# Optimization experiments

Measured on AMD Instinct MI355X. Metric: run time of the kernel, lower is better.

The kernel has to match this reference:

```python
import jax, jax.numpy as jnp
import numpy as np

NEG_INF = -1e25


def setup_inputs() -> dict:
    key = jax.random.key(0)
    ks = jax.random.split(key, 7)
    B, L, Q, H = 4, 512, 64, 768
    bert = jax.random.normal(ks[0], (B, L, H), dtype=jnp.float32)
    query = jax.random.normal(ks[1], (B, Q, H), dtype=jnp.float32)
    mask = jax.random.randint(ks[2], (B, L), 0, 2).astype(bool)
    # nn.Linear(2H, H): weight (H, 2H), bias (H)
    W_w = jax.random.normal(ks[3], (H, 2 * H), dtype=jnp.float32) * (1.0 / np.sqrt(2 * H))
    W_b = jax.random.normal(ks[4], (H,), dtype=jnp.float32) * 0.02
    # nn.Linear(H, 1): weight (1, H), bias (1)
    v_w = jax.random.normal(ks[5], (1, H), dtype=jnp.float32) * (1.0 / np.sqrt(H))
    v_b = jax.random.normal(ks[6], (1,), dtype=jnp.float32) * 0.02
    return {"bert": bert, "query": query, "mask": mask,
            "W_w": W_w, "W_b": W_b, "v_w": v_w, "v_b": v_b}


def reference(bert, query, mask, W_w, W_b, v_w, v_b):
    H = bert.shape[-1]
    # Linear(cat([bert, query])) = bert @ Wb^T + query @ Wq^T + b  (avoids the (B,Q,L,2H) concat)
    W_bert = W_w[:, :H]    # (H, H) acts on bert part
    W_query = W_w[:, H:]   # (H, H) acts on query part
    bp = jnp.einsum('blh,kh->blk', bert, W_bert)     # (B, L, H)
    qp = jnp.einsum('bqh,kh->bqk', query, W_query)   # (B, Q, H)
    h = jnp.tanh(bp[:, None, :, :] + qp[:, :, None, :] + W_b)  # (B, Q, L, H)
    x = jnp.einsum('bqlh,h->bql', h, v_w[0]) + v_b[0]           # (B, Q, L)
    x = jnp.where(mask[:, None, :], x, NEG_INF)
    return jax.nn.softmax(x, axis=-1)
```

## Files before the change

### kernel.cpp

```cpp
#include <hip/hip_runtime.h>
#include <hip/hip_bf16.h>

#define LOG2E    1.4426950408889634f
#define TWOLOG2E 2.8853900817779268f

typedef short bf16x8 __attribute__((ext_vector_type(8)));
typedef float f32x4  __attribute__((ext_vector_type(4)));
typedef unsigned short u16x8 __attribute__((ext_vector_type(8)));

static __device__ __forceinline__ float bf16_to_f(unsigned short u) {
    union { unsigned int i; float f; } v; v.i = ((unsigned int)u) << 16; return v.f;
}
static __device__ __forceinline__ unsigned short f_to_bf16_rne(float x) {
    union { float f; unsigned int i; } v; v.f = x;
    unsigned int lsb = (v.i >> 16) & 1u;
    v.i += 0x7fffu + lsb;
    return (unsigned short)(v.i >> 16);
}

__global__ __launch_bounds__(256) void cast_frag(
    const float* __restrict__ bert, const float* __restrict__ query,
    const float* __restrict__ Ww,
    unsigned short* __restrict__ Ahf, unsigned short* __restrict__ Alf,
    unsigned short* __restrict__ Whf, unsigned short* __restrict__ Wlf)
{
    const int i    = blockIdx.x * 256 + threadIdx.x;
    const int lane = i & 63;
    const float* src;
    float scale;
    unsigned short *dh, *dl;
    size_t di;
    if (i < 221184) {
        const int rest = i >> 6;
        const int kt = rest % 24, mt = rest / 24;
        const int m  = mt * 16 + (lane & 15);
        src = ((m < 2048) ? bert + (size_t)m * 768
                          : query + (size_t)(m - 2048) * 768)
              + kt * 32 + (lane >> 4) * 8;
        scale = 1.0f;
        dh = Ahf; dl = Alf; di = (size_t)i * 8;
    } else {
        const int j = i - 221184;
        const int rest = j >> 6;
        const int kt = rest % 24, nt2 = rest / 24;
        const int sel = (nt2 >= 48) ? 1 : 0;
        const int n   = (nt2 - sel * 48) * 16 + (lane & 15);
        src = Ww + (size_t)n * 1536 + sel * 768 + kt * 32 + (lane >> 4) * 8;
        scale = TWOLOG2E;
        dh = Whf; dl = Wlf; di = (size_t)j * 8;
    }
    float4 x0 = *(const float4*)src;
    float4 x1 = *(const float4*)(src + 4);
    float xs[8] = {x0.x * scale, x0.y * scale, x0.z * scale, x0.w * scale,
                   x1.x * scale, x1.y * scale, x1.z * scale, x1.w * scale};
    u16x8 h, l;
    #pragma unroll
    for (int e = 0; e < 8; ++e) {
        unsigned short hh = f_to_bf16_rne(xs[e]);
        h[e] = hh;
        l[e] = f_to_bf16_rne(xs[e] - bf16_to_f(hh));
    }
    *(u16x8*)(dh + di) = h;
    *(u16x8*)(dl + di) = l;
}

__global__ __launch_bounds__(64) void gemm_frag(
    const unsigned short* __restrict__ Ahf, const unsigned short* __restrict__ Alf,
    const unsigned short* __restrict__ Whf, const unsigned short* __restrict__ Wlf,
    const float* __restrict__ Wb, float* __restrict__ bpT, float* __restrict__ qp)
{
    const int l    = threadIdx.x;
    const int w    = blockIdx.x;
    const int mt_w = w / 24;
    const int nt_w = w % 24;
    const int m0   = mt_w * 32;
    const int n0   = nt_w * 32;
    const bool isq = (m0 >= 2048);
    const int  fmt = mt_w * 2;
    const int  fnt = (isq ? 48 : 0) + nt_w * 2;
    const int  lr  = l & 15;
    const int  kg  = l >> 4;

    const unsigned short* pAh = Ahf + (size_t)fmt * 12288 + l * 8;
    const unsigned short* pAl = Alf + (size_t)fmt * 12288 + l * 8;
    const unsigned short* pBh = Whf + (size_t)fnt * 12288 + l * 8;
    const unsigned short* pBl = Wlf + (size_t)fnt * 12288 + l * 8;

    f32x4 acc[2][2];
    #pragma unroll
    for (int i = 0; i < 2; ++i)
        #pragma unroll
        for (int j = 0; j < 2; ++j) acc[i][j] = (f32x4){0.f, 0.f, 0.f, 0.f};

    if (!isq) {
        #pragma unroll 4
        for (int kt = 0; kt < 24; ++kt) {
            bf16x8 ah[2], al[2], bh[2], bl[2];
            #pragma unroll
            for (int i = 0; i < 2; ++i) {
                ah[i] = *(const bf16x8*)(pAh + (size_t)i * 12288 + kt * 512);
                al[i] = *(const bf16x8*)(pAl + (size_t)i * 12288 + kt * 512);
                bh[i] = *(const bf16x8*)(pBh + (size_t)i * 12288 + kt * 512);
                bl[i] = *(const bf16x8*)(pBl + (size_t)i * 12288 + kt * 512);
            }
            #pragma unroll
            for (int i = 0; i < 2; ++i)
                #pragma unroll
                for (int j = 0; j < 2; ++j) {
                    acc[i][j] = __builtin_amdgcn_mfma_f32_16x16x32_bf16(bh[i], ah[j], acc[i][j], 0, 0, 0);
                    acc[i][j] = __builtin_amdgcn_mfma_f32_16x16x32_bf16(bh[i], al[j], acc[i][j], 0, 0, 0);
                    acc[i][j] = __builtin_amdgcn_mfma_f32_16x16x32_bf16(bl[i], ah[j], acc[i][j], 0, 0, 0);
                }
        }
        #pragma unroll
        for (int i = 0; i < 2; ++i)
            #pragma unroll
            for (int j = 0; j < 2; ++j)
                #pragma unroll
                for (int r = 0; r < 4; ++r) {
                    const int nrow = n0 + i * 16 + kg * 4 + r;
                    const int mcol = m0 + j * 16 + lr;
                    bpT[(size_t)nrow * 2048 + mcol] = acc[i][j][r];
                }
    } else {
        #pragma unroll 4
        for (int kt = 0; kt < 24; ++kt) {
            bf16x8 ah[2], al[2], bh[2], bl[2];
            #pragma unroll
            for (int i = 0; i < 2; ++i) {
                ah[i] = *(const bf16x8*)(pAh + (size_t)i * 12288 + kt * 512);
                al[i] = *(const bf16x8*)(pAl + (size_t)i * 12288 + kt * 512);
                bh[i] = *(const bf16x8*)(pBh + (size_t)i * 12288 + kt * 512);
                bl[i] = *(const bf16x8*)(pBl + (size_t)i * 12288 + kt * 512);
            }
            #pragma unroll
            for (int i = 0; i < 2; ++i)
                #pragma unroll
                for (int j = 0; j < 2; ++j) {
                    acc[i][j] = __builtin_amdgcn_mfma_f32_16x16x32_bf16(ah[i], bh[j], acc[i][j], 0, 0, 0);
                    acc[i][j] = __builtin_amdgcn_mfma_f32_16x16x32_bf16(ah[i], bl[j], acc[i][j], 0, 0, 0);
                    acc[i][j] = __builtin_amdgcn_mfma_f32_16x16x32_bf16(al[i], bh[j], acc[i][j], 0, 0, 0);
                }
        }
        #pragma unroll
        for (int j = 0; j < 2; ++j) {
            const int col  = n0 + j * 16 + lr;
            const float bias = Wb[col] * TWOLOG2E;
            #pragma unroll
            for (int i = 0; i < 2; ++i)
                #pragma unroll
                for (int r = 0; r < 4; ++r) {
                    const int row = m0 - 2048 + i * 16 + kg * 4 + r;
                    qp[(size_t)row * 768 + col] = acc[i][j][r] + bias;
                }
        }
    }
}

__global__ __launch_bounds__(128) void attn_dense(
    const float* __restrict__ bpT, const float* __restrict__ qp,
    const float* __restrict__ v_w, float* __restrict__ Xp)
{
    const int t  = threadIdx.x;
    const int bq = blockIdx.x;
    const int ks = blockIdx.y;
    const int b  = bq >> 6;
    const int k0 = ks * 96;
    const float* bT = bpT + (size_t)b * 512 + t * 4;
    const float* pq = qp + (size_t)bq * 768;
    f32x4 acc = {0.f, 0.f, 0.f, 0.f};
    #pragma unroll 4
    for (int k = k0; k < k0 + 96; ++k) {
        float4 bv = *(const float4*)(bT + (size_t)k * 2048);
        const float qk = pq[k];
        const float vk = v_w[k];
        acc[0] = fmaf(vk, __builtin_amdgcn_rcpf(1.0f + __builtin_amdgcn_exp2f(bv.x + qk)), acc[0]);
        acc[1] = fmaf(vk, __builtin_amdgcn_rcpf(1.0f + __builtin_amdgcn_exp2f(bv.y + qk)), acc[1]);
        acc[2] = fmaf(vk, __builtin_amdgcn_rcpf(1.0f + __builtin_amdgcn_exp2f(bv.z + qk)), acc[2]);
        acc[3] = fmaf(vk, __builtin_amdgcn_rcpf(1.0f + __builtin_amdgcn_exp2f(bv.w + qk)), acc[3]);
    }
    *(f32x4*)(Xp + (size_t)ks * 131072 + (size_t)bq * 512 + t * 4) = acc;
}

__global__ __launch_bounds__(512) void softmax_mask(
    const float* __restrict__ Xp, const int* __restrict__ mask,
    float* __restrict__ out)
{
    const int bq  = blockIdx.x;
    const int b   = bq >> 6;
    const int l   = threadIdx.x;
    const int wid = l >> 6;
    __shared__ float red[8];

    const size_t idx = (size_t)bq * 512 + l;
    float v = 0.f;
    #pragma unroll
    for (int p = 0; p < 8; ++p) v += Xp[idx + (size_t)p * 131072];
    v *= -2.f;
    const bool mk = (mask[b * 512 + l] != 0);
    v = mk ? v : -1e25f;

    float m = v;
    #pragma unroll
    for (int o = 32; o; o >>= 1) m = fmaxf(m, __shfl_xor(m, o));
    if ((l & 63) == 0) red[wid] = m;
    __syncthreads();
    #pragma unroll
    for (int i = 0; i < 8; ++i) m = fmaxf(m, red[i]);

    float e = __builtin_amdgcn_exp2f((v - m) * LOG2E);
    float s = e;
    #pragma unroll
    for (int o = 32; o; o >>= 1) s += __shfl_xor(s, o);
    __syncthreads();
    if ((l & 63) == 0) red[wid] = s;
    __syncthreads();
    s = 0.f;
    #pragma unroll
    for (int i = 0; i < 8; ++i) s += red[i];

    out[idx] = e / s;
}

extern "C" void kernel_launch(void* const* d_in, const int* in_sizes, int n_in,
                              void* d_out, int out_size, void* d_ws, size_t ws_size,
                              hipStream_t stream)
{
    const float* bert  = (const float*)d_in[0];
    const float* query = (const float*)d_in[1];
    const int*   mask  = (const int*)  d_in[2];
    const float* W_w   = (const float*)d_in[3];
    const float* W_b   = (const float*)d_in[4];
    const float* v_w   = (const float*)d_in[5];
    const float* v_b   = (const float*)d_in[6];
    (void)v_b;

    float* bpT = (float*)d_ws;
    float* qp  = bpT + (size_t)768 * 2048;
    float* Xp  = qp  + (size_t)256 * 768;
    unsigned short* Ahf = (unsigned short*)(Xp + (size_t)8 * 256 * 512);
    unsigned short* Alf = Ahf + (size_t)2304 * 768;
    unsigned short* Whf = Alf + (size_t)2304 * 768;
    unsigned short* Wlf = Whf + (size_t)1536 * 768;
    float* out = (float*)d_out;

    cast_frag<<<1440, 256, 0, stream>>>(bert, query, W_w, Ahf, Alf, Whf, Wlf);
    gemm_frag<<<1728, 64, 0, stream>>>(Ahf, Alf, Whf, Wlf, W_b, bpT, qp);
    attn_dense<<<dim3(256, 8), 128, 0, stream>>>(bpT, qp, v_w, Xp);
    softmax_mask<<<dim3(256), 512, 0, stream>>>(Xp, mask, out);
}
```

Baseline: 130.4 us.

## Stage GEMM tiles through LDS and process four queries per attention thread

Result: faster. 118.7 us (-8.9%).

```diff
diff --git a/kernel.cpp b/kernel.cpp
--- a/kernel.cpp
+++ b/kernel.cpp
@@ -64,27 +64,40 @@
     *(u16x8*)(dl + di) = l;
 }
 
-__global__ __launch_bounds__(64) void gemm_frag(
+__global__ __launch_bounds__(256) void gemm_lds(
     const unsigned short* __restrict__ Ahf, const unsigned short* __restrict__ Alf,
     const unsigned short* __restrict__ Whf, const unsigned short* __restrict__ Wlf,
     const float* __restrict__ Wb, float* __restrict__ bpT, float* __restrict__ qp)
 {
-    const int l    = threadIdx.x;
-    const int w    = blockIdx.x;
-    const int mt_w = w / 24;
-    const int nt_w = w % 24;
-    const int m0   = mt_w * 32;
-    const int n0   = nt_w * 32;
-    const bool isq = (m0 >= 2048);
-    const int  fmt = mt_w * 2;
-    const int  fnt = (isq ? 48 : 0) + nt_w * 2;
-    const int  lr  = l & 15;
-    const int  kg  = l >> 4;
-
-    const unsigned short* pAh = Ahf + (size_t)fmt * 12288 + l * 8;
-    const unsigned short* pAl = Alf + (size_t)fmt * 12288 + l * 8;
-    const unsigned short* pBh = Whf + (size_t)fnt * 12288 + l * 8;
-    const unsigned short* pBl = Wlf + (size_t)fnt * 12288 + l * 8;
+    __shared__ short lds[8192];
+
+    const int t    = threadIdx.x;
+    const int w    = t >> 6;
+    const int lane = t & 63;
+    const int wi   = w >> 1;
+    const int wj   = w & 1;
+    const int lr   = lane & 15;
+    const int kg   = lane >> 4;
+
+    const int blk  = blockIdx.x;
+    const int mt2  = blk / 12;
+    const int nt2  = blk % 12;
+    const bool isq = (mt2 >= 32);
+    const int fmtA = mt2 * 4;
+    const int fntB = (isq ? 48 : 0) + nt2 * 4;
+
+    const unsigned short* gsrc[4];
+    #pragma unroll
+    for (int c = 0; c < 4; ++c) {
+        const int r = w * 4 + c;
+        if (r < 8) {
+            const int f = r >> 1;
+            gsrc[c] = ((r & 1) ? Alf : Ahf) + (size_t)(fmtA + f) * 12288 + lane * 8;
+        } else {
+            const int f = (r - 8) >> 1;
+            gsrc[c] = ((r & 1) ? Wlf : Whf) + (size_t)(fntB + f) * 12288 + lane * 8;
+        }
+    }
 
     f32x4 acc[2][2];
     #pragma unroll
@@ -92,94 +105,114 @@
         #pragma unroll
         for (int j = 0; j < 2; ++j) acc[i][j] = (f32x4){0.f, 0.f, 0.f, 0.f};
 
+    for (int kt = 0; kt < 24; ++kt) {
+        #pragma unroll
+        for (int c = 0; c < 4; ++c) {
+            const int r = w * 4 + c;
+            __builtin_amdgcn_global_load_lds(
+                (const __attribute__((address_space(1))) unsigned int*)(gsrc[c] + kt * 512),
+                (__attribute__((address_space(3))) unsigned int*)&lds[r * 512],
+                16, 0, 0);
+        }
+        __syncthreads();
+
+        bf16x8 ah[2], al[2], bh[2], bl[2];
+        #pragma unroll
+        for (int ii = 0; ii < 2; ++ii) {
+            const int a = 2 * wi + ii;
+            ah[ii] = *(const bf16x8*)&lds[(a * 2 + 0) * 512 + lane * 8];
+            al[ii] = *(const bf16x8*)&lds[(a * 2 + 1) * 512 + lane * 8];
+        }
+        #pragma unroll
+        for (int jj = 0; jj < 2; ++jj) {
+            const int b = 2 * wj + jj;
+            bh[jj] = *(const bf16x8*)&lds[4096 + (b * 2 + 0) * 512 + lane * 8];
+            bl[jj] = *(const bf16x8*)&lds[4096 + (b * 2 + 1) * 512 + lane * 8];
+        }
+
+        if (!isq) {
+            #pragma unroll
+            for (int ii = 0; ii < 2; ++ii)
+                #pragma unroll
+                for (int jj = 0; jj < 2; ++jj) {
+                    acc[ii][jj] = __builtin_amdgcn_mfma_f32_16x16x32_bf16(bh[jj], ah[ii], acc[ii][jj], 0, 0, 0);
+                    acc[ii][jj] = __builtin_amdgcn_mfma_f32_16x16x32_bf16(bh[jj], al[ii], acc[ii][jj], 0, 0, 0);
+                    acc[ii][jj] = __builtin_amdgcn_mfma_f32_16x16x32_bf16(bl[jj], ah[ii], acc[ii][jj], 0, 0, 0);
+                }
+        } else {
+            #pragma unroll
+            for (int ii = 0; ii < 2; ++ii)
+                #pragma unroll
+                for (int jj = 0; jj < 2; ++jj) {
+                    acc[ii][jj] = __builtin_amdgcn_mfma_f32_16x16x32_bf16(ah[ii], bh[jj], acc[ii][jj], 0, 0, 0);
+                    acc[ii][jj] = __builtin_amdgcn_mfma_f32_16x16x32_bf16(ah[ii], bl[jj], acc[ii][jj], 0, 0, 0);
+                    acc[ii][jj] = __builtin_amdgcn_mfma_f32_16x16x32_bf16(al[ii], bh[jj], acc[ii][jj], 0, 0, 0);
+                }
+        }
+        __syncthreads();
+    }
+
+    const int m0 = mt2 * 64 + wi * 32;
+    const int n0 = nt2 * 64 + wj * 32;
     if (!isq) {
-        #pragma unroll 4
-        for (int kt = 0; kt < 24; ++kt) {
-            bf16x8 ah[2], al[2], bh[2], bl[2];
-            #pragma unroll
-            for (int i = 0; i < 2; ++i) {
-                ah[i] = *(const bf16x8*)(pAh + (size_t)i * 12288 + kt * 512);
-                al[i] = *(const bf16x8*)(pAl + (size_t)i * 12288 + kt * 512);
-                bh[i] = *(const bf16x8*)(pBh + (size_t)i * 12288 + kt * 512);
-                bl[i] = *(const bf16x8*)(pBl + (size_t)i * 12288 + kt * 512);
-            }
-            #pragma unroll
-            for (int i = 0; i < 2; ++i)
-                #pragma unroll
-                for (int j = 0; j < 2; ++j) {
-                    acc[i][j] = __builtin_amdgcn_mfma_f32_16x16x32_bf16(bh[i], ah[j], acc[i][j], 0, 0, 0);
-                    acc[i][j] = __builtin_amdgcn_mfma_f32_16x16x32_bf16(bh[i], al[j], acc[i][j], 0, 0, 0);
-                    acc[i][j] = __builtin_amdgcn_mfma_f32_16x16x32_bf16(bl[i], ah[j], acc[i][j], 0, 0, 0);
-                }
-        }
-        #pragma unroll
-        for (int i = 0; i < 2; ++i)
-            #pragma unroll
-            for (int j = 0; j < 2; ++j)
+        #pragma unroll
+        for (int ii = 0; ii < 2; ++ii)
+            #pragma unroll
+            for (int jj = 0; jj < 2; ++jj)
                 #pragma unroll
                 for (int r = 0; r < 4; ++r) {
-                    const int nrow = n0 + i * 16 + kg * 4 + r;
-                    const int mcol = m0 + j * 16 + lr;
-                    bpT[(size_t)nrow * 2048 + mcol] = acc[i][j][r];
+                    const int nrow = n0 + jj * 16 + kg * 4 + r;
+                    const int mcol = m0 + ii * 16 + lr;
+                    bpT[(size_t)nrow * 2048 + mcol] = acc[ii][jj][r];
                 }
     } else {
-        #pragma unroll 4
-        for (int kt = 0; kt < 24; ++kt) {
-            bf16x8 ah[2], al[2], bh[2], bl[2];
-            #pragma unroll
-            for (int i = 0; i < 2; ++i) {
-                ah[i] = *(const bf16x8*)(pAh + (size_t)i * 12288 + kt * 512);
-                al[i] = *(const bf16x8*)(pAl + (size_t)i * 12288 + kt * 512);
-                bh[i] = *(const bf16x8*)(pBh + (size_t)i * 12288 + kt * 512);
-                bl[i] = *(const bf16x8*)(pBl + (size_t)i * 12288 + kt * 512);
-            }
-            #pragma unroll
-            for (int i = 0; i < 2; ++i)
-                #pragma unroll
-                for (int j = 0; j < 2; ++j) {
-                    acc[i][j] = __builtin_amdgcn_mfma_f32_16x16x32_bf16(ah[i], bh[j], acc[i][j], 0, 0, 0);
-                    acc[i][j] = __builtin_amdgcn_mfma_f32_16x16x32_bf16(ah[i], bl[j], acc[i][j], 0, 0, 0);
-                    acc[i][j] = __builtin_amdgcn_mfma_f32_16x16x32_bf16(al[i], bh[j], acc[i][j], 0, 0, 0);
-                }
-        }
-        #pragma unroll
-        for (int j = 0; j < 2; ++j) {
-            const int col  = n0 + j * 16 + lr;
+        #pragma unroll
+        for (int jj = 0; jj < 2; ++jj) {
+            const int col  = n0 + jj * 16 + lr;
             const float bias = Wb[col] * TWOLOG2E;
             #pragma unroll
-            for (int i = 0; i < 2; ++i)
+            for (int ii = 0; ii < 2; ++ii)
                 #pragma unroll
                 for (int r = 0; r < 4; ++r) {
-                    const int row = m0 - 2048 + i * 16 + kg * 4 + r;
-                    qp[(size_t)row * 768 + col] = acc[i][j][r] + bias;
-                }
-        }
-    }
-}
-
-__global__ __launch_bounds__(128) void attn_dense(
+                    const int row = m0 - 2048 + ii * 16 + kg * 4 + r;
+                    qp[(size_t)row * 768 + col] = acc[ii][jj][r] + bias;
+                }
+        }
+    }
+}
+
+__global__ __launch_bounds__(128) void attn_dense4(
     const float* __restrict__ bpT, const float* __restrict__ qp,
     const float* __restrict__ v_w, float* __restrict__ Xp)
 {
-    const int t  = threadIdx.x;
-    const int bq = blockIdx.x;
-    const int ks = blockIdx.y;
-    const int b  = bq >> 6;
-    const int k0 = ks * 96;
+    const int t   = threadIdx.x;
+    const int bqt = blockIdx.x;
+    const int ks  = blockIdx.y;
+    const int b   = bqt >> 4;
+    const int q0  = (bqt & 15) * 4;
+    const int k0  = ks * 48;
     const float* bT = bpT + (size_t)b * 512 + t * 4;
-    const float* pq = qp + (size_t)bq * 768;
-    f32x4 acc = {0.f, 0.f, 0.f, 0.f};
+    const float* pq = qp + (size_t)(b * 64 + q0) * 768;
+    f32x4 acc[4];
+    #pragma unroll
+    for (int qi = 0; qi < 4; ++qi) acc[qi] = (f32x4){0.f, 0.f, 0.f, 0.f};
+
     #pragma unroll 4
-    for (int k = k0; k < k0 + 96; ++k) {
+    for (int k = k0; k < k0 + 48; ++k) {
         float4 bv = *(const float4*)(bT + (size_t)k * 2048);
-        const float qk = pq[k];
         const float vk = v_w[k];
-        acc[0] = fmaf(vk, __builtin_amdgcn_rcpf(1.0f + __builtin_amdgcn_exp2f(bv.x + qk)), acc[0]);
-        acc[1] = fmaf(vk, __builtin_amdgcn_rcpf(1.0f + __builtin_amdgcn_exp2f(bv.y + qk)), acc[1]);
-        acc[2] = fmaf(vk, __builtin_amdgcn_rcpf(1.0f + __builtin_amdgcn_exp2f(bv.z + qk)), acc[2]);
-        acc[3] = fmaf(vk, __builtin_amdgcn_rcpf(1.0f + __builtin_amdgcn_exp2f(bv.w + qk)), acc[3]);
-    }
-    *(f32x4*)(Xp + (size_t)ks * 131072 + (size_t)bq * 512 + t * 4) = acc;
+        float qk[4] = {pq[k], pq[768 + k], pq[1536 + k], pq[2304 + k]};
+        #pragma unroll
+        for (int qi = 0; qi < 4; ++qi) {
+            acc[qi][0] = fmaf(vk, __builtin_amdgcn_rcpf(1.0f + __builtin_amdgcn_exp2f(bv.x + qk[qi])), acc[qi][0]);
+            acc[qi][1] = fmaf(vk, __builtin_amdgcn_rcpf(1.0f + __builtin_amdgcn_exp2f(bv.y + qk[qi])), acc[qi][1]);
+            acc[qi][2] = fmaf(vk, __builtin_amdgcn_rcpf(1.0f + __builtin_amdgcn_exp2f(bv.z + qk[qi])), acc[qi][2]);
+            acc[qi][3] = fmaf(vk, __builtin_amdgcn_rcpf(1.0f + __builtin_amdgcn_exp2f(bv.w + qk[qi])), acc[qi][3]);
+        }
+    }
+    #pragma unroll
+    for (int qi = 0; qi < 4; ++qi)
+        *(f32x4*)(Xp + (size_t)ks * 131072 + (size_t)(b * 64 + q0 + qi) * 512 + t * 4) = acc[qi];
 }
 
 __global__ __launch_bounds__(512) void softmax_mask(
@@ -195,7 +228,7 @@
     const size_t idx = (size_t)bq * 512 + l;
     float v = 0.f;
     #pragma unroll
-    for (int p = 0; p < 8; ++p) v += Xp[idx + (size_t)p * 131072];
+    for (int p = 0; p < 16; ++p) v += Xp[idx + (size_t)p * 131072];
     v *= -2.f;
     const bool mk = (mask[b * 512 + l] != 0);
     v = mk ? v : -1e25f;
@@ -238,14 +271,14 @@
     float* bpT = (float*)d_ws;
     float* qp  = bpT + (size_t)768 * 2048;
     float* Xp  = qp  + (size_t)256 * 768;
-    unsigned short* Ahf = (unsigned short*)(Xp + (size_t)8 * 256 * 512);
+    unsigned short* Ahf = (unsigned short*)(Xp + (size_t)16 * 256 * 512);
     unsigned short* Alf = Ahf + (size_t)2304 * 768;
     unsigned short* Whf = Alf + (size_t)2304 * 768;
     unsigned short* Wlf = Whf + (size_t)1536 * 768;
     float* out = (float*)d_out;
 
     cast_frag<<<1440, 256, 0, stream>>>(bert, query, W_w, Ahf, Alf, Whf, Wlf);
-    gemm_frag<<<1728, 64, 0, stream>>>(Ahf, Alf, Whf, Wlf, W_b, bpT, qp);
-    attn_dense<<<dim3(256, 8), 128, 0, stream>>>(bpT, qp, v_w, Xp);
+    gemm_lds<<<432, 256, 0, stream>>>(Ahf, Alf, Whf, Wlf, W_b, bpT, qp);
+    attn_dense4<<<dim3(64, 16), 128, 0, stream>>>(bpT, qp, v_w, Xp);
     softmax_mask<<<dim3(256), 512, 0, stream>>>(Xp, mask, out);
 }
```
